# Kernel tuning notes

Hardware: AMD Instinct MI355X
Metric: run time of the kernel (lower is better)

The kernel has to match this reference:

```python
import jax, jax.numpy as jnp
import numpy as np

B, T, D = 256, 500, 3   # batch, time steps, input features (time, mag, err)
U, C = 512, 10          # PhasedLSTM units, n_classes
R_ON = 0.05             # open ratio of the phased time gate
ALPHA = 1e-3            # leak rate during closed phase
LN_EPS = 1e-3           # keras LayerNormalization default epsilon


def _glorot(key, shape):
    lim = np.sqrt(6.0 / (shape[0] + shape[1])).astype(np.float32)
    return jax.random.uniform(key, shape, jnp.float32, -lim, lim)


def setup_inputs() -> dict:
    key = jax.random.key(0)
    ks = jax.random.split(key, 12)
    x = jax.random.normal(ks[0], (B, T, D), jnp.float32)
    # monotonically increasing observation times per sample
    times = jnp.cumsum(jax.random.uniform(ks[1], (B, T), jnp.float32), axis=1)
    # layer 0 PhasedLSTM params (gate order i, f, g, o)
    W0 = _glorot(ks[2], (D, 4 * U)); R0 = _glorot(ks[3], (U, 4 * U)); b0 = jnp.zeros((4 * U,), jnp.float32)
    tau0 = jnp.exp(jax.random.uniform(ks[4], (U,), jnp.float32, 0.0, 3.0))
    s0 = jax.random.uniform(ks[5], (U,), jnp.float32) * tau0
    # layer 1
    W1 = _glorot(ks[6], (U, 4 * U)); R1 = _glorot(ks[7], (U, 4 * U)); b1 = jnp.zeros((4 * U,), jnp.float32)
    tau1 = jnp.exp(jax.random.uniform(ks[8], (U,), jnp.float32, 0.0, 3.0))
    s1 = jax.random.uniform(ks[9], (U,), jnp.float32) * tau1
    # per-layer LayerNorm params
    g0 = jnp.ones((U,), jnp.float32); be0 = jnp.zeros((U,), jnp.float32)
    g1 = jnp.ones((U,), jnp.float32); be1 = jnp.zeros((U,), jnp.float32)
    # classifier head
    Wf = _glorot(ks[10], (U, C)); bf = jnp.zeros((C,), jnp.float32)
    return dict(x=x, times=times, W0=W0, R0=R0, b0=b0, tau0=tau0, s0=s0, g0=g0, be0=be0,
                W1=W1, R1=R1, b1=b1, tau1=tau1, s1=s1, g1=g1, be1=be1, Wf=Wf, bf=bf)


def _layernorm(h, g, b):
    m = jnp.mean(h, axis=-1, keepdims=True)
    v = jnp.var(h, axis=-1, keepdims=True)
    return (h - m) * jax.lax.rsqrt(v + LN_EPS) * g + b


def _time_gate(t, tau, s):
    # t: [B], tau/s: [U] -> k: [B, U]
    phi = jnp.mod(t[:, None] - s, tau) / tau
    return jnp.where(phi < 0.5 * R_ON, 2.0 * phi / R_ON,
                     jnp.where(phi < R_ON, 2.0 - 2.0 * phi / R_ON, ALPHA * phi))


def _plstm_step(xi, ti, h, c, W, R, b, tau, s):
    z = xi @ W + h @ R + b                       # [B, 4U]
    i, f, g, o = jnp.split(z, 4, axis=-1)
    i = jax.nn.sigmoid(i); f = jax.nn.sigmoid(f); o = jax.nn.sigmoid(o)
    c_new = f * c + i * jnp.tanh(g)
    h_new = o * jnp.tanh(c_new)
    k = _time_gate(ti, tau, s)                   # phased time gate
    return k * h_new + (1.0 - k) * h, k * c_new + (1.0 - k) * c


def reference(x, times, W0, R0, b0, tau0, s0, g0, be0,
              W1, R1, b1, tau1, s1, g1, be1, Wf, bf):
    xt = jnp.transpose(x, (1, 0, 2))  # [T, B, D]
    tt = times.T                      # [T, B]
    zeros = jnp.zeros((x.shape[0], U), x.dtype)
    init = (zeros, zeros, zeros, zeros)

    def step(carry, inp):
        h0, c0, h1, c1 = carry
        xi, ti = inp
        h0n, c0n = _plstm_step(xi, ti, h0, c0, W0, R0, b0, tau0, s0)
        a0 = _layernorm(h0n, g0, be0)   # normed output feeds next layer; raw state is carried
        h1n, c1n = _plstm_step(a0, ti, h1, c1, W1, R1, b1, tau1, s1)
        a1 = _layernorm(h1n, g1, be1)
        probs = jax.nn.softmax(a1 @ Wf + bf)  # dropout is identity at inference
        return (h0n, c0n, h1n, c1n), probs

    _, out = jax.lax.scan(step, init, (xt, tt))  # out: [T, B, C]
    return jnp.transpose(out, (1, 0, 2))
```

## Files before the change

kernel.cpp:

```cpp
#include <hip/hip_runtime.h>
#include <hip/hip_bf16.h>


#define NB 256
#define NTHR 512
#define T_STEPS 500
#define RON 0.05f
#define ALPHA_LEAK 1e-3f

typedef short short8 __attribute__((ext_vector_type(8)));
typedef float f32x4 __attribute__((ext_vector_type(4)));
typedef unsigned long long ull;

#define OFF_WSWZ 0u
#define OFF_U1   6291456u
#define OFF_V1   6299648u
#define OFF_WFP  6307840u
#define OFF_UFV  6328320u
#define OFF_H0B  6328448u
#define OFF_H1B  6852736u
#define OFF_ST0  7377024u
#define OFF_ST1  7508096u
#define OFF_FLG0 7639168u
#define OFF_FLG1 7640192u
#define ZERO_BYTES 1312768u

#define SMEM_BYTES 147968

#define AT_LD(p)    __hip_atomic_load((p), __ATOMIC_RELAXED, __HIP_MEMORY_SCOPE_AGENT)
#define AT_ST(p, v) __hip_atomic_store((p), (v), __ATOMIC_RELAXED, __HIP_MEMORY_SCOPE_AGENT)

#define G2L(gp, lp) \
  __builtin_amdgcn_global_load_lds( \
      (const __attribute__((address_space(1))) void*)(gp), \
      (__attribute__((address_space(3))) void*)(lp), 16, 0, 16)

__device__ __forceinline__ short f2bf(float x) {
  unsigned u = __float_as_uint(x);
  unsigned r = (u + 0x7fffu + ((u >> 16) & 1u)) >> 16;
  return (short)r;
}
__device__ __forceinline__ float bf2f(short s) {
  return __uint_as_float(((unsigned)(unsigned short)s) << 16);
}
__device__ __forceinline__ float sigm(float x) { return 1.f / (1.f + __expf(-x)); }
__device__ __forceinline__ float tanh_f(float x) {
  float cx = fminf(fmaxf(x, -15.f), 15.f);
  float e = __expf(2.f * cx);
  return (e - 1.f) / (e + 1.f);
}
__device__ __forceinline__ float timegate(float t, float tau, float s) {
  float phi = fmodf(t - s, tau);
  if (phi < 0.f) phi += tau;
  phi /= tau;
  return phi < 0.5f * RON ? (2.f / RON) * phi
       : (phi < RON ? 2.f - (2.f / RON) * phi : ALPHA_LEAK * phi);
}
__device__ __forceinline__ int fragidx(int m, int k) {
  return ((((k >> 5) * 2 + (m >> 4)) * 64) + (((k >> 3) & 3) * 16) + (m & 15)) * 8 + (k & 7);
}

__global__ void prep_weights(const float* __restrict__ R0, const float* __restrict__ W1,
                             const float* __restrict__ R1, const float* __restrict__ g0,
                             short* __restrict__ Wswz) {
  int t = blockIdx.x * 256 + threadIdx.x;
  int lane = t & 63; int rest = t >> 6;
  int nf = rest & 1;  rest >>= 1;
  int kb = rest & 15; rest >>= 4;
  int ch = rest & 1;  rest >>= 1;
  int mm = rest % 3;  int slice = rest / 3;
  int c = ch * 32 + nf * 16 + (lane & 15);
  int gate = c >> 4;
  int unit = slice * 16 + (c & 15);
  int gcol = gate * 512 + unit;
  int k0 = kb * 32 + (lane >> 4) * 8;
  const float* src = (mm == 0) ? R0 : (mm == 1 ? W1 : R1);
  short8 o;
  #pragma unroll
  for (int e = 0; e < 8; ++e) {
    float v = src[(size_t)(k0 + e) * 2048 + gcol];
    if (mm == 1) v *= g0[k0 + e];
    o[e] = f2bf(v);
  }
  *(short8*)(Wswz + (size_t)t * 8) = o;
}

__global__ void prep_vecs(const float* __restrict__ W1, const float* __restrict__ g0,
                          const float* __restrict__ be0,
                          float* __restrict__ u1, float* __restrict__ v1) {
  int c = blockIdx.x * 256 + threadIdx.x;
  float su = 0.f, sv = 0.f;
  for (int k = 0; k < 512; ++k) {
    float w = W1[(size_t)k * 2048 + c];
    su += be0[k] * w; sv += g0[k] * w;
  }
  u1[c] = su; v1[c] = sv;
}

__global__ void prep_head(const float* __restrict__ Wf, const float* __restrict__ g1,
                          const float* __restrict__ be1, const float* __restrict__ bfv,
                          float* __restrict__ Wfp, float* __restrict__ ufv) {
  int t = blockIdx.x * 256 + threadIdx.x;
  if (t < 5120) {
    int kk = t / 640, rem = t - kk * 640, c = rem >> 6, l = rem & 63;
    int k = 8 * l + kk;
    Wfp[t] = g1[k] * Wf[k * 10 + c];
  }
  if (t < 10) {
    float su = bfv[t], sv = 0.f;
    for (int k = 0; k < 512; ++k) {
      float w = Wf[k * 10 + t];
      su += be1[k] * w; sv += g1[k] * w;
    }
    ufv[t] = su; ufv[16 + t] = sv;
  }
}

struct Ptrs {
  const float *x, *times, *W0, *b0, *tau0, *s0, *b1, *tau1, *s1;
  const float *u1v, *v1v, *Wfp, *ufv;
  short *H0b, *H1b;
  float *St0, *St1;
  unsigned *flag0, *flag1;
  float *out;
};

__launch_bounds__(NTHR, 1)
__global__ void plstm_persist(Ptrs P, const short* __restrict__ Wswz) {
  extern __shared__ char smem[];
  short* h0b  = (short*)smem;
  short* h1bL = (short*)(smem + 32768);
  float* zbv  = (float*)(smem + 98304);
  float* mus  = (float*)(smem + 124032);
  float* xtb  = (float*)(smem + 124544);
  float* prm  = (float*)(smem + 125184);
  float* wfl  = (float*)(smem + 127232);
  float* ufl  = (float*)(smem + 147712);

  const int tid = threadIdx.x;
  const int g = blockIdx.x & 7;
  const int slice = blockIdx.x >> 3;
  const int wid = tid >> 6, lane = tid & 63;
  const int mm = wid >> 1, ch = wid & 1;
  const int gm0 = g * 32;

  for (int i = tid; i < 512; i += NTHR) {
    float v;
    if (i < 192)      { int f = i >> 6, c = i & 63; v = P.W0[f * 2048 + ((c >> 4) << 9) + slice * 16 + (c & 15)]; }
    else if (i < 256) { int c = i & 63; v = P.b0[((c >> 4) << 9) + slice * 16 + (c & 15)]; }
    else if (i < 320) { int c = i & 63; int gc = ((c >> 4) << 9) + slice * 16 + (c & 15);
                        v = P.b1[gc] + P.u1v[gc]; }
    else if (i < 384) { int c = i & 63; v = P.v1v[((c >> 4) << 9) + slice * 16 + (c & 15)]; }
    else if (i < 448) v = 0.f;
    else if (i < 464) v = P.tau0[slice * 16 + (i & 15)];
    else if (i < 480) v = P.s0[slice * 16 + (i & 15)];
    else if (i < 496) v = P.tau1[slice * 16 + (i & 15)];
    else              v = P.s1[slice * 16 + (i & 15)];
    prm[i] = v;
  }
  for (int i = tid; i < 5120; i += NTHR) wfl[i] = P.Wfp[i];
  if (tid < 32) ufl[tid] = P.ufv[tid];

  short8 wr[16][2];
  if (wid < 6) {
    const short* wb = Wswz + ((((size_t)slice * 3 + mm) * 2 + ch) * 32 * 64) * 8;
    #pragma unroll
    for (int kb = 0; kb < 16; ++kb)
      #pragma unroll
      for (int nf = 0; nf < 2; ++nf) {
        wr[kb][nf] = *(const short8*)(wb + ((kb * 2 + nf) * 64 + lane) * 8);
        asm volatile("" : "+v"(wr[kb][nf]));
      }
  }
  float hS0 = 0.f, hS1 = 0.f, cS0 = 0.f, cS1 = 0.f;
  __syncthreads();

  for (int r = 0; r <= T_STEPS + 1; ++r) {
    const int bufA = (r + 1) & 1;
    const int bufB = r & 1;
    short* h1s = h1bL + bufB * 16384;

    if (wid == 0) {
      { const unsigned tgt = (unsigned)r;
        const unsigned* fp = P.flag0 + g * 32 + (lane & 31);
        for (int it_ = 0; it_ < 200000; ++it_) {
          unsigned v = (lane < 32) ? AT_LD(fp) : 0xFFFFFFFFu;
          if (__all((int)(v >= tgt))) break;
          __builtin_amdgcn_s_sleep(1);
        } }
      const char* gA = (const char*)(P.H0b + ((size_t)bufA * 8 + g) * 16384);
      const char* gB = (const char*)(P.H1b + ((size_t)bufB * 8 + g) * 16384);
      char* lA = (char*)h0b;
      char* lB = (char*)h1s;
      #pragma unroll
      for (int j = 0; j < 32; ++j) {
        unsigned off = j * 1024u + (unsigned)lane * 16u;
        G2L(gA + off, lA + off);
        G2L(gB + off, lB + off);
      }
    } else if (wid == 6) {
      { const unsigned tgt = (unsigned)r;
        const unsigned* fp = P.flag0 + g * 32 + (lane & 31);
        for (int it_ = 0; it_ < 200000; ++it_) {
          unsigned v = (lane < 32) ? AT_LD(fp) : 0xFFFFFFFFu;
          if (__all((int)(v >= tgt))) break;
          __builtin_amdgcn_s_sleep(1);
        } }
      const int layer = lane >> 5, m = lane & 31;
      const float* base = layer ? (P.St1 + ((size_t)bufB * 8 + g) * 2048 + m * 64)
                                : (P.St0 + ((size_t)bufA * 8 + g) * 2048 + m * 64);
      const ull* bu = (const ull*)base;
      float s_ = 0.f, q_ = 0.f;
      #pragma unroll
      for (int sl = 0; sl < 32; ++sl) {
        ull v = AT_LD(bu + sl);
        s_ += __uint_as_float((unsigned)v);
        q_ += __uint_as_float((unsigned)(v >> 32));
      }
      float mu = s_ * (1.f / 512.f);
      float var = q_ * (1.f / 512.f) - mu * mu;
      mus[layer * 64 + m] = mu;
      mus[layer * 64 + 32 + m] = rsqrtf(var + 1e-3f);
    } else if (wid == 7) {
      int m = lane & 31;
      if (lane < 32) {
        int step = (r < T_STEPS) ? r : (T_STEPS - 1);
        const float* xp = P.x + ((size_t)(gm0 + m) * T_STEPS + step) * 3;
        xtb[m * 4 + 0] = xp[0]; xtb[m * 4 + 1] = xp[1]; xtb[m * 4 + 2] = xp[2];
        xtb[m * 4 + 3] = P.times[(size_t)(gm0 + m) * T_STEPS + step];
      } else {
        int s1_ = (r >= 1) ? r - 1 : 0;
        if (s1_ > T_STEPS - 1) s1_ = T_STEPS - 1;
        xtb[128 + m] = P.times[(size_t)(gm0 + m) * T_STEPS + s1_];
      }
    }
    __syncthreads();
    float m1r = 0.f, r1r = 0.f;
    if (wid == 7) { m1r = mus[64 + slice]; r1r = mus[96 + slice]; }

    if (wid < 6 && r <= T_STEPS) {
      f32x4 acc[2][2] = {};
      const short* asrc = (mm == 2) ? h1s : h0b;
      #pragma unroll
      for (int kb = 0; kb < 16; ++kb) {
        short8 a0 = *(const short8*)(asrc + ((kb * 2 + 0) * 64 + lane) * 8);
        short8 a1 = *(const short8*)(asrc + ((kb * 2 + 1) * 64 + lane) * 8);
        #pragma unroll
        for (int nf = 0; nf < 2; ++nf) {
          acc[0][nf] = __builtin_amdgcn_mfma_f32_16x16x32_bf16(a0, wr[kb][nf], acc[0][nf], 0, 0, 0);
          acc[1][nf] = __builtin_amdgcn_mfma_f32_16x16x32_bf16(a1, wr[kb][nf], acc[1][nf], 0, 0, 0);
        }
      }
      float* z = zbv + mm * 2144;
      #pragma unroll
      for (int mf = 0; mf < 2; ++mf)
        #pragma unroll
        for (int nf = 0; nf < 2; ++nf)
          #pragma unroll
          for (int q = 0; q < 4; ++q) {
            int row = mf * 16 + (lane >> 4) * 4 + q;
            int col = ch * 32 + nf * 16 + (lane & 15);
            z[row * 67 + col] = acc[mf][nf][q];
          }
    }
    __syncthreads();

    {
      const bool isL0 = (tid < 256);
      const bool act = isL0 ? (r < T_STEPS) : (r >= 1 && r <= T_STEPS);
      if (act) {
        const int idx = isL0 ? tid : (tid - 256);
        const int m = idx >> 3, u0 = (idx & 7) << 1;
        unsigned pack = 0; float hnv[2];
        if (isL0) {
          float x0 = xtb[m * 4], x1 = xtb[m * 4 + 1], x2 = xtb[m * 4 + 2];
          float tmv = xtb[m * 4 + 3];
          #pragma unroll
          for (int uu = 0; uu < 2; ++uu) {
            int u = u0 + uu;
            float zg[4];
            #pragma unroll
            for (int q = 0; q < 4; ++q) {
              int c = q * 16 + u;
              zg[q] = zbv[m * 67 + c] + prm[192 + c]
                    + x0 * prm[c] + x1 * prm[64 + c] + x2 * prm[128 + c];
            }
            float iv = sigm(zg[0]), fv = sigm(zg[1]), gv = tanh_f(zg[2]), ov = sigm(zg[3]);
            float cold = uu ? cS1 : cS0, hold = uu ? hS1 : hS0;
            float cp = fv * cold + iv * gv;
            float hp = ov * tanh_f(cp);
            float k = timegate(tmv, prm[448 + u], prm[464 + u]);
            float hn = k * hp + (1.f - k) * hold;
            float cn = k * cp + (1.f - k) * cold;
            if (uu) { hS1 = hn; cS1 = cn; } else { hS0 = hn; cS0 = cn; }
            hnv[uu] = hn;
            pack |= ((unsigned)(unsigned short)f2bf(hn)) << (16 * uu);
          }
          AT_ST((unsigned*)(P.H0b + ((size_t)bufB * 8 + g) * 16384 + fragidx(m, slice * 16 + u0)), pack);
        } else {
          float mu0m = mus[m], rs0m = mus[32 + m];
          float tmv = xtb[128 + m];
          #pragma unroll
          for (int uu = 0; uu < 2; ++uu) {
            int u = u0 + uu;
            float zg[4];
            #pragma unroll
            for (int q = 0; q < 4; ++q) {
              int c = q * 16 + u;
              float zA = zbv[2144 + m * 67 + c];
              float zB = zbv[4288 + m * 67 + c];
              zg[q] = rs0m * zA + zB + prm[256 + c] - mu0m * rs0m * prm[320 + c];
            }
            float iv = sigm(zg[0]), fv = sigm(zg[1]), gv = tanh_f(zg[2]), ov = sigm(zg[3]);
            float cold = uu ? cS1 : cS0, hold = uu ? hS1 : hS0;
            float cp = fv * cold + iv * gv;
            float hp = ov * tanh_f(cp);
            float k = timegate(tmv, prm[480 + u], prm[496 + u]);
            float hn = k * hp + (1.f - k) * hold;
            float cn = k * cp + (1.f - k) * cold;
            if (uu) { hS1 = hn; cS1 = cn; } else { hS0 = hn; cS0 = cn; }
            hnv[uu] = hn;
            pack |= ((unsigned)(unsigned short)f2bf(hn)) << (16 * uu);
          }
          AT_ST((unsigned*)(P.H1b + ((size_t)bufA * 8 + g) * 16384 + fragidx(m, slice * 16 + u0)), pack);
        }
        float sr = hnv[0] + hnv[1], qr = hnv[0] * hnv[0] + hnv[1] * hnv[1];
        sr += __shfl_down(sr, 4, 8); qr += __shfl_down(qr, 4, 8);
        sr += __shfl_down(sr, 2, 8); qr += __shfl_down(qr, 2, 8);
        sr += __shfl_down(sr, 1, 8); qr += __shfl_down(qr, 1, 8);
        if ((idx & 7) == 0) {
          ull pv = ((ull)__float_as_uint(qr) << 32) | __float_as_uint(sr);
          ull* sp = isL0
              ? ((ull*)(P.St0 + ((size_t)bufB * 8 + g) * 2048) + m * 32 + slice)
              : ((ull*)(P.St1 + ((size_t)bufA * 8 + g) * 2048) + m * 32 + slice);
          AT_ST(sp, pv);
        }
      }
    }
    __syncthreads();

    if (tid == 0 && r <= T_STEPS) {
      AT_ST(P.flag0 + g * 32 + slice, (unsigned)(r + 1));
    }
    if (wid == 7 && r >= 2) {
      const int msam = slice;
      short8 hv8 = *(const short8*)(h1s + fragidx(msam, lane * 8));
      float lg[10];
      #pragma unroll
      for (int c = 0; c < 10; ++c) lg[c] = 0.f;
      #pragma unroll
      for (int kk = 0; kk < 8; ++kk) {
        float hv = bf2f(hv8[kk]);
        const float* wf = wfl + kk * 640 + lane;
        #pragma unroll
        for (int c = 0; c < 10; ++c) lg[c] += hv * wf[c * 64];
      }
      #pragma unroll
      for (int off = 32; off > 0; off >>= 1)
        #pragma unroll
        for (int c = 0; c < 10; ++c) lg[c] += __shfl_down(lg[c], off, 64);
      if (lane == 0) {
        float logit[10], mx = -1e30f;
        #pragma unroll
        for (int c = 0; c < 10; ++c) {
          logit[c] = r1r * lg[c] + ufl[c] - m1r * r1r * ufl[16 + c];
          mx = fmaxf(mx, logit[c]);
        }
        float ssum = 0.f;
        #pragma unroll
        for (int c = 0; c < 10; ++c) { logit[c] = expf(logit[c] - mx); ssum += logit[c]; }
        float inv = 1.f / ssum;
        float* op = P.out + ((size_t)(gm0 + msam) * T_STEPS + (r - 2)) * 10;
        #pragma unroll
        for (int c = 0; c < 10; ++c) op[c] = logit[c] * inv;
      }
    }
  }
}

extern "C" void kernel_launch(void* const* d_in, const int* in_sizes, int n_in,
                              void* d_out, int out_size, void* d_ws, size_t ws_size,
                              hipStream_t stream) {
  const float* x    = (const float*)d_in[0];
  const float* tms  = (const float*)d_in[1];
  const float* W0   = (const float*)d_in[2];
  const float* R0   = (const float*)d_in[3];
  const float* b0   = (const float*)d_in[4];
  const float* tau0 = (const float*)d_in[5];
  const float* s0   = (const float*)d_in[6];
  const float* g0   = (const float*)d_in[7];
  const float* be0  = (const float*)d_in[8];
  const float* W1   = (const float*)d_in[9];
  const float* R1   = (const float*)d_in[10];
  const float* b1   = (const float*)d_in[11];
  const float* tau1 = (const float*)d_in[12];
  const float* s1   = (const float*)d_in[13];
  const float* g1   = (const float*)d_in[14];
  const float* be1  = (const float*)d_in[15];
  const float* Wf   = (const float*)d_in[16];
  const float* bfv  = (const float*)d_in[17];

  char* ws = (char*)d_ws;
  short* Wswz = (short*)(ws + OFF_WSWZ);
  float* u1m  = (float*)(ws + OFF_U1);
  float* v1m  = (float*)(ws + OFF_V1);
  float* Wfpm = (float*)(ws + OFF_WFP);
  float* ufvm = (float*)(ws + OFF_UFV);

  Ptrs P;
  P.x = x; P.times = tms; P.W0 = W0; P.b0 = b0; P.tau0 = tau0; P.s0 = s0;
  P.b1 = b1; P.tau1 = tau1; P.s1 = s1;
  P.u1v = u1m; P.v1v = v1m; P.Wfp = Wfpm; P.ufv = ufvm;
  P.H0b = (short*)(ws + OFF_H0B);
  P.H1b = (short*)(ws + OFF_H1B);
  P.St0 = (float*)(ws + OFF_ST0);
  P.St1 = (float*)(ws + OFF_ST1);
  P.flag0 = (unsigned*)(ws + OFF_FLG0);
  P.flag1 = (unsigned*)(ws + OFF_FLG1);
  P.out = (float*)d_out;

  hipFuncSetAttribute(reinterpret_cast<const void*>(plstm_persist),
                      hipFuncAttributeMaxDynamicSharedMemorySize, SMEM_BYTES);

  prep_weights<<<1536, 256, 0, stream>>>(R0, W1, R1, g0, Wswz);
  prep_vecs<<<8, 256, 0, stream>>>(W1, g0, be0, u1m, v1m);
  prep_head<<<20, 256, 0, stream>>>(Wf, g1, be1, bfv, Wfpm, ufvm);
  hipMemsetAsync(ws + OFF_H0B, 0, ZERO_BYTES, stream);
  plstm_persist<<<NB, NTHR, SMEM_BYTES, stream>>>(P, Wswz);
}
```

Baseline: 5.900 ms.

## Shrink block to six waves and split per-layer flags with LDS token handoffs

Cuts the persistent block from eight waves to six, so every wave runs MFMA and the idle helper waves are folded into loader and stat roles. The single per-group flag is split into separate layer-0 and layer-1 flags. Each loader wave waits only on the flag for the data it copies, and LDS tokens order the waves inside the block. The trailing __syncthreads before the flag publish is replaced by per-layer LDS counters, so layer 0 can signal readiness without waiting for layer 1. In exchange it adds more spin loops and finer-grained ordering, which makes the code fragile and may raise per-wave register pressure.

```diff
diff --git a/kernel.cpp b/kernel.cpp
--- a/kernel.cpp
+++ b/kernel.cpp
@@ -3,7 +3,7 @@
 
 
 #define NB 256
-#define NTHR 512
+#define NTHR 384
 #define T_STEPS 500
 #define RON 0.05f
 #define ALPHA_LEAK 1e-3f
@@ -29,6 +29,9 @@
 
 #define AT_LD(p)    __hip_atomic_load((p), __ATOMIC_RELAXED, __HIP_MEMORY_SCOPE_AGENT)
 #define AT_ST(p, v) __hip_atomic_store((p), (v), __ATOMIC_RELAXED, __HIP_MEMORY_SCOPE_AGENT)
+#define LDS_ADD(p)  __hip_atomic_fetch_add((p), 1u, __ATOMIC_RELEASE, __HIP_MEMORY_SCOPE_WORKGROUP)
+#define LDS_LD(p)   __hip_atomic_load((p), __ATOMIC_ACQUIRE, __HIP_MEMORY_SCOPE_WORKGROUP)
+#define LDS_ST(p,v) __hip_atomic_store((p), (v), __ATOMIC_RELEASE, __HIP_MEMORY_SCOPE_WORKGROUP)
 
 #define G2L(gp, lp) \
   __builtin_amdgcn_global_load_lds( \
@@ -136,6 +139,7 @@
   float* prm  = (float*)(smem + 125184);
   float* wfl  = (float*)(smem + 127232);
   float* ufl  = (float*)(smem + 147712);
+  unsigned* tok = (unsigned*)(smem + 147840);
 
   const int tid = threadIdx.x;
   const int g = blockIdx.x & 7;
@@ -144,6 +148,7 @@
   const int mm = wid >> 1, ch = wid & 1;
   const int gm0 = g * 32;
 
+  if (tid < 4) tok[tid] = 0u;
   for (int i = tid; i < 512; i += NTHR) {
     float v;
     if (i < 192)      { int f = i >> 6, c = i & 63; v = P.W0[f * 2048 + ((c >> 4) << 9) + slice * 16 + (c & 15)]; }
@@ -162,7 +167,7 @@
   if (tid < 32) ufl[tid] = P.ufv[tid];
 
   short8 wr[16][2];
-  if (wid < 6) {
+  {
     const short* wb = Wswz + ((((size_t)slice * 3 + mm) * 2 + ch) * 32 * 64) * 8;
     #pragma unroll
     for (int kb = 0; kb < 16; ++kb)
@@ -172,7 +177,9 @@
         asm volatile("" : "+v"(wr[kb][nf]));
       }
   }
-  float hS0 = 0.f, hS1 = 0.f, cS0 = 0.f, cS1 = 0.f;
+  float h0A0 = 0.f, h0A1 = 0.f, c0A0 = 0.f, c0A1 = 0.f;
+  float h1S[4] = {0.f, 0.f, 0.f, 0.f};
+  float c1S[4] = {0.f, 0.f, 0.f, 0.f};
   __syncthreads();
 
   for (int r = 0; r <= T_STEPS + 1; ++r) {
@@ -188,22 +195,74 @@
           if (__all((int)(v >= tgt))) break;
           __builtin_amdgcn_s_sleep(1);
         } }
+      if (lane == 0) LDS_ST(&tok[0], (unsigned)(r + 1));
       const char* gA = (const char*)(P.H0b + ((size_t)bufA * 8 + g) * 16384);
-      const char* gB = (const char*)(P.H1b + ((size_t)bufB * 8 + g) * 16384);
       char* lA = (char*)h0b;
-      char* lB = (char*)h1s;
-      #pragma unroll
-      for (int j = 0; j < 32; ++j) {
-        unsigned off = j * 1024u + (unsigned)lane * 16u;
+      #pragma unroll
+      for (int j = 0; j < 16; ++j) {
+        unsigned off = (unsigned)(j * 64 + lane) * 16u;
         G2L(gA + off, lA + off);
-        G2L(gB + off, lB + off);
-      }
-    } else if (wid == 6) {
-      { const unsigned tgt = (unsigned)r;
-        const unsigned* fp = P.flag0 + g * 32 + (lane & 31);
+      }
+    } else if (wid == 1) {
+      { const unsigned tgt = (unsigned)(r + 1);
+        for (int it_ = 0; it_ < 2000000; ++it_) {
+          if (LDS_LD(&tok[0]) >= tgt) break;
+          __builtin_amdgcn_s_sleep(1);
+        } }
+      const char* gA = (const char*)(P.H0b + ((size_t)bufA * 8 + g) * 16384) + 16384;
+      char* lA = (char*)h0b + 16384;
+      #pragma unroll
+      for (int j = 0; j < 16; ++j) {
+        unsigned off = (unsigned)(j * 64 + lane) * 16u;
+        G2L(gA + off, lA + off);
+      }
+    } else if (wid == 2) {
+      { const unsigned tgt = (unsigned)((r >= 2) ? r : 0);
+        const unsigned* fp = P.flag1 + g * 32 + (lane & 31);
         for (int it_ = 0; it_ < 200000; ++it_) {
           unsigned v = (lane < 32) ? AT_LD(fp) : 0xFFFFFFFFu;
           if (__all((int)(v >= tgt))) break;
+          __builtin_amdgcn_s_sleep(1);
+        } }
+      if (lane == 0) LDS_ST(&tok[1], (unsigned)(r + 1));
+      const char* gB = (const char*)(P.H1b + ((size_t)bufB * 8 + g) * 16384);
+      char* lB = (char*)h1s;
+      #pragma unroll
+      for (int j = 0; j < 16; ++j) {
+        unsigned off = (unsigned)(j * 64 + lane) * 16u;
+        G2L(gB + off, lB + off);
+      }
+    } else if (wid == 3) {
+      { const unsigned tgt = (unsigned)(r + 1);
+        for (int it_ = 0; it_ < 2000000; ++it_) {
+          if (LDS_LD(&tok[1]) >= tgt) break;
+          __builtin_amdgcn_s_sleep(1);
+        } }
+      const char* gB = (const char*)(P.H1b + ((size_t)bufB * 8 + g) * 16384) + 16384;
+      char* lB = (char*)h1s + 16384;
+      #pragma unroll
+      for (int j = 0; j < 16; ++j) {
+        unsigned off = (unsigned)(j * 64 + lane) * 16u;
+        G2L(gB + off, lB + off);
+      }
+    } else if (wid == 4) {
+      int m = lane & 31;
+      if (lane < 32) {
+        int step = (r < T_STEPS) ? r : (T_STEPS - 1);
+        const float* xp = P.x + ((size_t)(gm0 + m) * T_STEPS + step) * 3;
+        xtb[m * 4 + 0] = xp[0];
+        xtb[m * 4 + 1] = xp[1];
+        xtb[m * 4 + 2] = xp[2];
+        xtb[m * 4 + 3] = P.times[(size_t)(gm0 + m) * T_STEPS + step];
+      } else {
+        int s1_ = (r >= 1) ? (r - 1) : 0;
+        if (s1_ > T_STEPS - 1) s1_ = T_STEPS - 1;
+        xtb[128 + m] = P.times[(size_t)(gm0 + m) * T_STEPS + s1_];
+      }
+    } else {
+      { const unsigned tgt = (unsigned)(r + 1);
+        for (int it_ = 0; it_ < 2000000; ++it_) {
+          if (LDS_LD(&tok[0]) >= tgt && LDS_LD(&tok[1]) >= tgt) break;
           __builtin_amdgcn_s_sleep(1);
         } }
       const int layer = lane >> 5, m = lane & 31;
@@ -221,24 +280,12 @@
       float var = q_ * (1.f / 512.f) - mu * mu;
       mus[layer * 64 + m] = mu;
       mus[layer * 64 + 32 + m] = rsqrtf(var + 1e-3f);
-    } else if (wid == 7) {
-      int m = lane & 31;
-      if (lane < 32) {
-        int step = (r < T_STEPS) ? r : (T_STEPS - 1);
-        const float* xp = P.x + ((size_t)(gm0 + m) * T_STEPS + step) * 3;
-        xtb[m * 4 + 0] = xp[0]; xtb[m * 4 + 1] = xp[1]; xtb[m * 4 + 2] = xp[2];
-        xtb[m * 4 + 3] = P.times[(size_t)(gm0 + m) * T_STEPS + step];
-      } else {
-        int s1_ = (r >= 1) ? r - 1 : 0;
-        if (s1_ > T_STEPS - 1) s1_ = T_STEPS - 1;
-        xtb[128 + m] = P.times[(size_t)(gm0 + m) * T_STEPS + s1_];
-      }
     }
     __syncthreads();
     float m1r = 0.f, r1r = 0.f;
-    if (wid == 7) { m1r = mus[64 + slice]; r1r = mus[96 + slice]; }
-
-    if (wid < 6 && r <= T_STEPS) {
+    if (wid == 1) { m1r = mus[64 + slice]; r1r = mus[96 + slice]; }
+
+    if (r <= T_STEPS) {
       f32x4 acc[2][2] = {};
       const short* asrc = (mm == 2) ? h1s : h0b;
       #pragma unroll
@@ -265,85 +312,107 @@
     }
     __syncthreads();
 
-    {
-      const bool isL0 = (tid < 256);
-      const bool act = isL0 ? (r < T_STEPS) : (r >= 1 && r <= T_STEPS);
-      if (act) {
-        const int idx = isL0 ? tid : (tid - 256);
-        const int m = idx >> 3, u0 = (idx & 7) << 1;
+    const bool l0act = (r < T_STEPS);
+    const bool l1act = (r >= 1 && r <= T_STEPS);
+    if (tid < 256) {
+      if (l0act) {
+        int m = tid >> 3, u0 = (tid & 7) << 1;
+        float x0 = xtb[m * 4 + 0], x1 = xtb[m * 4 + 1], x2 = xtb[m * 4 + 2];
+        float tmv = xtb[m * 4 + 3];
         unsigned pack = 0; float hnv[2];
-        if (isL0) {
-          float x0 = xtb[m * 4], x1 = xtb[m * 4 + 1], x2 = xtb[m * 4 + 2];
-          float tmv = xtb[m * 4 + 3];
+        #pragma unroll
+        for (int uu = 0; uu < 2; ++uu) {
+          int u = u0 + uu;
+          float zg[4];
           #pragma unroll
-          for (int uu = 0; uu < 2; ++uu) {
-            int u = u0 + uu;
-            float zg[4];
-            #pragma unroll
-            for (int q = 0; q < 4; ++q) {
-              int c = q * 16 + u;
-              zg[q] = zbv[m * 67 + c] + prm[192 + c]
-                    + x0 * prm[c] + x1 * prm[64 + c] + x2 * prm[128 + c];
-            }
-            float iv = sigm(zg[0]), fv = sigm(zg[1]), gv = tanh_f(zg[2]), ov = sigm(zg[3]);
-            float cold = uu ? cS1 : cS0, hold = uu ? hS1 : hS0;
-            float cp = fv * cold + iv * gv;
-            float hp = ov * tanh_f(cp);
-            float k = timegate(tmv, prm[448 + u], prm[464 + u]);
-            float hn = k * hp + (1.f - k) * hold;
-            float cn = k * cp + (1.f - k) * cold;
-            if (uu) { hS1 = hn; cS1 = cn; } else { hS0 = hn; cS0 = cn; }
-            hnv[uu] = hn;
-            pack |= ((unsigned)(unsigned short)f2bf(hn)) << (16 * uu);
+          for (int q = 0; q < 4; ++q) {
+            int c = q * 16 + u;
+            zg[q] = zbv[m * 67 + c] + prm[192 + c]
+                  + x0 * prm[c] + x1 * prm[64 + c] + x2 * prm[128 + c];
           }
-          AT_ST((unsigned*)(P.H0b + ((size_t)bufB * 8 + g) * 16384 + fragidx(m, slice * 16 + u0)), pack);
-        } else {
-          float mu0m = mus[m], rs0m = mus[32 + m];
-          float tmv = xtb[128 + m];
-          #pragma unroll
-          for (int uu = 0; uu < 2; ++uu) {
-            int u = u0 + uu;
-            float zg[4];
-            #pragma unroll
-            for (int q = 0; q < 4; ++q) {
-              int c = q * 16 + u;
-              float zA = zbv[2144 + m * 67 + c];
-              float zB = zbv[4288 + m * 67 + c];
-              zg[q] = rs0m * zA + zB + prm[256 + c] - mu0m * rs0m * prm[320 + c];
-            }
-            float iv = sigm(zg[0]), fv = sigm(zg[1]), gv = tanh_f(zg[2]), ov = sigm(zg[3]);
-            float cold = uu ? cS1 : cS0, hold = uu ? hS1 : hS0;
-            float cp = fv * cold + iv * gv;
-            float hp = ov * tanh_f(cp);
-            float k = timegate(tmv, prm[480 + u], prm[496 + u]);
-            float hn = k * hp + (1.f - k) * hold;
-            float cn = k * cp + (1.f - k) * cold;
-            if (uu) { hS1 = hn; cS1 = cn; } else { hS0 = hn; cS0 = cn; }
-            hnv[uu] = hn;
-            pack |= ((unsigned)(unsigned short)f2bf(hn)) << (16 * uu);
-          }
-          AT_ST((unsigned*)(P.H1b + ((size_t)bufA * 8 + g) * 16384 + fragidx(m, slice * 16 + u0)), pack);
-        }
+          float iv = sigm(zg[0]), fv = sigm(zg[1]), gv = tanh_f(zg[2]), ov = sigm(zg[3]);
+          float cold = uu ? c0A1 : c0A0, hold = uu ? h0A1 : h0A0;
+          float cp = fv * cold + iv * gv;
+          float hp = ov * tanh_f(cp);
+          float k = timegate(tmv, prm[448 + u], prm[464 + u]);
+          float hn = k * hp + (1.f - k) * hold;
+          float cn = k * cp + (1.f - k) * cold;
+          if (uu) { h0A1 = hn; c0A1 = cn; } else { h0A0 = hn; c0A0 = cn; }
+          hnv[uu] = hn;
+          pack |= ((unsigned)(unsigned short)f2bf(hn)) << (16 * uu);
+        }
+        AT_ST((unsigned*)(P.H0b + ((size_t)bufB * 8 + g) * 16384 + fragidx(m, slice * 16 + u0)), pack);
         float sr = hnv[0] + hnv[1], qr = hnv[0] * hnv[0] + hnv[1] * hnv[1];
         sr += __shfl_down(sr, 4, 8); qr += __shfl_down(qr, 4, 8);
         sr += __shfl_down(sr, 2, 8); qr += __shfl_down(qr, 2, 8);
         sr += __shfl_down(sr, 1, 8); qr += __shfl_down(qr, 1, 8);
-        if ((idx & 7) == 0) {
+        if ((tid & 7) == 0) {
           ull pv = ((ull)__float_as_uint(qr) << 32) | __float_as_uint(sr);
-          ull* sp = isL0
-              ? ((ull*)(P.St0 + ((size_t)bufB * 8 + g) * 2048) + m * 32 + slice)
-              : ((ull*)(P.St1 + ((size_t)bufA * 8 + g) * 2048) + m * 32 + slice);
-          AT_ST(sp, pv);
-        }
+          AT_ST((ull*)(P.St0 + ((size_t)bufB * 8 + g) * 2048) + m * 32 + slice, pv);
+        }
+      }
+      asm volatile("s_waitcnt vmcnt(0)" ::: "memory");
+      if (lane == 0) LDS_ADD(&tok[2]);
+      if (wid == 3 && lane == 0) {
+        const unsigned tgt = 4u * (unsigned)(r + 1);
+        for (int it_ = 0; it_ < 2000000; ++it_) {
+          if (LDS_LD(&tok[2]) >= tgt) break;
+          __builtin_amdgcn_s_sleep(1);
+        }
+        if (r <= T_STEPS) AT_ST(P.flag0 + g * 32 + slice, (unsigned)(r + 1));
+      }
+    } else {
+      if (l1act) {
+        int t = tid - 256;
+        int m = t >> 2, j = t & 3;
+        float mu0m = mus[m], rs0m = mus[32 + m];
+        float tmv = xtb[128 + m];
+        ull pack = 0;
+        float s_ = 0.f, q_ = 0.f;
+        #pragma unroll
+        for (int uu = 0; uu < 4; ++uu) {
+          int u = 4 * j + uu;
+          float zg[4];
+          #pragma unroll
+          for (int q = 0; q < 4; ++q) {
+            int c = q * 16 + u;
+            float zA = zbv[2144 + m * 67 + c];
+            float zB = zbv[4288 + m * 67 + c];
+            zg[q] = rs0m * zA + zB + prm[256 + c] - mu0m * rs0m * prm[320 + c];
+          }
+          float iv = sigm(zg[0]), fv = sigm(zg[1]), gv = tanh_f(zg[2]), ov = sigm(zg[3]);
+          float cold = c1S[uu], hold = h1S[uu];
+          float cp = fv * cold + iv * gv;
+          float hp = ov * tanh_f(cp);
+          float k = timegate(tmv, prm[480 + u], prm[496 + u]);
+          float hn = k * hp + (1.f - k) * hold;
+          float cn = k * cp + (1.f - k) * cold;
+          h1S[uu] = hn; c1S[uu] = cn;
+          s_ += hn; q_ += hn * hn;
+          pack |= ((ull)(unsigned short)f2bf(hn)) << (16 * uu);
+        }
+        AT_ST((ull*)(P.H1b + ((size_t)bufA * 8 + g) * 16384 + fragidx(m, slice * 16 + 4 * j)), pack);
+        s_ += __shfl_down(s_, 2, 4); q_ += __shfl_down(q_, 2, 4);
+        s_ += __shfl_down(s_, 1, 4); q_ += __shfl_down(q_, 1, 4);
+        if (j == 0) {
+          ull pv = ((ull)__float_as_uint(q_) << 32) | __float_as_uint(s_);
+          AT_ST((ull*)(P.St1 + ((size_t)bufA * 8 + g) * 2048) + m * 32 + slice, pv);
+        }
+      }
+      asm volatile("s_waitcnt vmcnt(0)" ::: "memory");
+      if (lane == 0) LDS_ADD(&tok[3]);
+      if (wid == 5 && lane == 0) {
+        const unsigned tgt = 2u * (unsigned)(r + 1);
+        for (int it_ = 0; it_ < 2000000; ++it_) {
+          if (LDS_LD(&tok[3]) >= tgt) break;
+          __builtin_amdgcn_s_sleep(1);
+        }
+        if (r >= 1 && r <= T_STEPS) AT_ST(P.flag1 + g * 32 + slice, (unsigned)(r + 1));
       }
     }
-    __syncthreads();
-
-    if (tid == 0 && r <= T_STEPS) {
-      AT_ST(P.flag0 + g * 32 + slice, (unsigned)(r + 1));
-    }
-    if (wid == 7 && r >= 2) {
-      const int msam = slice;
+
+    if (wid == 1 && r >= 2) {
+      int msam = slice;
       short8 hv8 = *(const short8*)(h1s + fragidx(msam, lane * 8));
       float lg[10];
       #pragma unroll
```

New measurement: 7.519 ms. 1.27x slower.
